# Performance work log

Hardware: AMD Instinct MI355X
Metric: run time of the kernel (lower is better)

The kernel has to match this reference:

```python
import jax, jax.numpy as jnp
import numpy as np

LAST_Q = 64      # queries used for dynamic pattern estimation (MInference default)
V_TOPK = 1024    # number of vertical (column) indices kept
S_TOPK = 2048    # number of slash (diagonal) offsets kept
FORCE_V = 30     # first columns always kept
FORCE_S = 100    # most-recent diagonals always kept


def setup_inputs() -> dict:
    key = jax.random.key(0)
    kq, kk, kv = jax.random.split(key, 3)
    B, H, S, D = 1, 8, 4096, 128
    q = jax.random.normal(kq, (B, H, S, D), dtype=jnp.float32)
    k = jax.random.normal(kk, (B, H, S, D), dtype=jnp.float32)
    v = jax.random.normal(kv, (B, H, S, D), dtype=jnp.float32)
    return {"q": q, "k": k, "v": v}


def _vertical_slash_attention(q, k, v):
    B, H, S, D = q.shape
    scale = 1.0 / np.sqrt(D).astype(np.float32)

    # ---- pattern estimation on the last LAST_Q queries ----
    qk = jnp.einsum('bhqd,bhkd->bhqk', q[:, :, -LAST_Q:], k) * scale  # [B,H,LQ,S]
    qpos = S - LAST_Q + jnp.arange(LAST_Q)                            # query positions
    causal_last = qpos[:, None] >= jnp.arange(S)[None, :]             # [LQ,S]
    qk = jnp.where(causal_last, qk, jnp.finfo(qk.dtype).min)
    qk = jax.nn.softmax(qk, axis=-1)

    # vertical (column) scores
    vertical = qk.sum(axis=2)                                         # [B,H,S]
    vertical = vertical.at[..., :FORCE_V].set(jnp.inf)
    v_idx = jax.lax.top_k(vertical, V_TOPK)[1]                        # column ids [B,H,V_TOPK]

    # slash (diagonal) scores, indexed by distance o = i - j in [0, S)
    dist = qpos[:, None] - jnp.arange(S)[None, :]                     # [LQ,S]
    dist_c = jnp.clip(dist, 0, S - 1)
    slash = jnp.zeros((B, H, S), qk.dtype).at[:, :, dist_c].add(
        jnp.where(dist >= 0, qk, 0.0))                                # [B,H,S]
    slash = slash.at[..., :FORCE_S].set(jnp.inf)
    s_off = jax.lax.top_k(slash, S_TOPK)[1]                           # diagonal offsets [B,H,S_TOPK]

    # ---- build vertical-slash sparsity mask ----
    ar = jnp.arange(S)
    v_mask = (v_idx[..., :, None] == ar).any(axis=-2)                 # [B,H,S] column allowed
    s_mask = (s_off[..., :, None] == ar).any(axis=-2)                 # [B,H,S] offset allowed

    dmat = ar[:, None] - ar[None, :]                                  # [S,S] query-key distance
    causal = dmat >= 0
    allowed = causal & (v_mask[:, :, None, :] | s_mask[:, :, jnp.clip(dmat, 0, S - 1)])

    # ---- sparse (mask-equivalent) attention ----
    scores = jnp.einsum('bhqd,bhkd->bhqk', q, k) * scale              # [B,H,S,S]
    scores = jnp.where(allowed, scores, jnp.finfo(scores.dtype).min)
    probs = jax.nn.softmax(scores, axis=-1)
    return jnp.einsum('bhqk,bhkd->bhqd', probs, v)


def reference(q, k, v):
    return _vertical_slash_attention(q, k, v)
```

## Files before the change

kernel.cpp:

```cpp
#include <hip/hip_runtime.h>
#include <hip/hip_bf16.h>
#include <math.h>

#define S_LEN 4096
#define DHEAD 128
#define NHEAD 8
#define LASTQ 64
#define V_TOPK 1024
#define S_TOPK 2048
#define FORCE_V 30
#define FORCE_S 100

#define SCALE 0.08838834764831845f
#define NEGBIG -3.0e38f

#define NJOBS 111

typedef __attribute__((ext_vector_type(8))) short short8;
typedef __attribute__((ext_vector_type(4))) float floatx4;
typedef unsigned long long u64;

__device__ __forceinline__ unsigned short f2bf(float f) {
    unsigned u = __float_as_uint(f);
    unsigned r = (u + 0x7fffu + ((u >> 16) & 1u)) >> 16;
    return (unsigned short)r;
}
__device__ __forceinline__ float bf2f(unsigned short s) {
    unsigned u = ((unsigned)s) << 16;
    return __uint_as_float(u);
}

__device__ const short jobQ[NJOBS] = {
    0,1,2,3,4, 5,5, 6,6, 7,7, 8,8, 9,9, 10,10,
    11,11,11, 12,12,12, 13,13,13, 14,14,14, 15,15,15,
    16,16,16,16, 17,17,17,17, 18,18,18,18, 19,19,19,19, 20,20,20,20, 21,21,21,21,
    22,22,22,22,22, 23,23,23,23,23, 24,24,24,24,24, 25,25,25,25,25, 26,26,26,26,26,
    27,27,27,27,27,27, 28,28,28,28,28,28, 29,29,29,29,29,29, 30,30,30,30,30,30,
    31,31,31,31,31,31};
__device__ const short jobK0[NJOBS] = {
    0,0,0,0,0, 0,6, 0,7, 0,8, 0,9, 0,10, 0,11,
    0,8,16, 0,9,18, 0,10,19, 0,10,20, 0,11,22,
    0,9,18,26, 0,9,18,27, 0,10,20,29, 0,10,20,30, 0,11,22,32, 0,11,22,33,
    0,10,19,28,37, 0,10,20,30,39, 0,10,20,30,40, 0,11,22,32,42, 0,11,22,33,44,
    0,10,20,29,38,47, 0,10,20,30,40,49, 0,10,20,30,40,50, 0,11,22,32,42,52,
    0,11,22,33,44,54};
__device__ const short jobK1[NJOBS] = {
    2,4,6,8,10, 6,12, 7,14, 8,16, 9,18, 10,20, 11,22,
    8,16,24, 9,18,26, 10,19,28, 10,20,30, 11,22,32,
    9,18,26,34, 9,18,27,36, 10,20,29,38, 10,20,30,40, 11,22,32,42, 11,22,33,44,
    10,19,28,37,46, 10,20,30,39,48, 10,20,30,40,50, 11,22,32,42,52, 11,22,33,44,54,
    10,20,29,38,47,56, 10,20,30,40,49,58, 10,20,30,40,50,60, 11,22,32,42,52,62,
    11,22,33,44,54,64};
__device__ const short pBase[32] = {0,1,2,3,4,5,7,9,11,13,15,17,20,23,26,29,
                                    32,36,40,44,48,52,56,61,66,71,76,81,87,93,99,105};
__device__ const short pCnt[32]  = {1,1,1,1,1,2,2,2,2,2,2,3,3,3,3,3,
                                    4,4,4,4,4,4,5,5,5,5,5,6,6,6,6,6};

__global__ __launch_bounds__(256) void prep_score(const float* __restrict__ q,
                                                  const float* __restrict__ k,
                                                  const float* __restrict__ v,
                                                  unsigned short* __restrict__ kbf,
                                                  unsigned short* __restrict__ vtbf,
                                                  float* __restrict__ scores) {
    int b = blockIdx.x, t = threadIdx.x;
    __shared__ __align__(16) float4 SH[64 * 32];

    if (b < 512) {
        const float4* src = (const float4*)k;
        int base = b * 2048;
#pragma unroll
        for (int i = 0; i < 8; ++i) {
            int idx = base + i * 256 + t;
            float4 val = src[idx];
            ushort4 o;
            o.x = f2bf(val.x); o.y = f2bf(val.y); o.z = f2bf(val.z); o.w = f2bf(val.w);
            ((ushort4*)kbf)[idx] = o;
        }
    } else if (b < 1536) {
        int bx = b - 512;
        int h  = bx >> 7;
        int rem = bx & 127;
        int d0 = (rem >> 6) * 64;
        int k0 = (rem & 63) * 64;
        unsigned short (*T)[72] = reinterpret_cast<unsigned short(*)[72]>(SH);
#pragma unroll
        for (int it = 0; it < 4; ++it) {
            int idx = t + it * 256;
            int r = idx >> 4, c4 = idx & 15;
            float4 val = *(const float4*)(v + ((size_t)(h * S_LEN) + k0 + r) * DHEAD + d0 + c4 * 4);
            T[c4 * 4 + 0][r] = f2bf(val.x);
            T[c4 * 4 + 1][r] = f2bf(val.y);
            T[c4 * 4 + 2][r] = f2bf(val.z);
            T[c4 * 4 + 3][r] = f2bf(val.w);
        }
        __syncthreads();
#pragma unroll
        for (int it = 0; it < 2; ++it) {
            int idx = t + it * 256;
            int r = idx >> 3, c8 = idx & 7;
            *(uint4*)(vtbf + ((size_t)h * DHEAD + d0 + r) * S_LEN + k0 + c8 * 8) = *(uint4*)&T[r][c8 * 8];
        }
    } else {
        int bx = b - 1536;
        int h  = bx >> 6;
        int kt = bx & 63;
        int jl = t >> 2, part = t & 3;
        int j  = kt * 64 + jl;

        float4* Qs = (float4*)SH;
        const float4* qbase = (const float4*)(q + ((size_t)h * S_LEN + (S_LEN - LASTQ)) * DHEAD);
        for (int idx = t; idx < 64 * 32; idx += 256) Qs[idx] = qbase[idx];
        __syncthreads();

        float4 kr[8];
        const float4* kp = (const float4*)(k + ((size_t)h * S_LEN + j) * DHEAD) + part * 8;
#pragma unroll
        for (int c = 0; c < 8; ++c) kr[c] = kp[c];

        float* sp = scores + (size_t)h * LASTQ * S_LEN + j;
#pragma unroll 4
        for (int qi = 0; qi < LASTQ; ++qi) {
            const float4* qp4 = Qs + qi * 32 + part * 8;
            float dot = 0.f;
#pragma unroll
            for (int c = 0; c < 8; ++c) {
                float4 a = qp4[c], bb = kr[c];
                dot += a.x * bb.x + a.y * bb.y + a.z * bb.z + a.w * bb.w;
            }
            dot += __shfl_xor(dot, 1, 64);
            dot += __shfl_xor(dot, 2, 64);
            if (part == 0) {
                int qpos = S_LEN - LASTQ + qi;
                sp[(size_t)qi * S_LEN] = (j <= qpos) ? dot * SCALE : NEGBIG;
            }
        }
    }
}

__global__ __launch_bounds__(256) void row_stats(const float* __restrict__ scores,
                                                 float* __restrict__ m_out,
                                                 float* __restrict__ inv_out) {
    int row  = blockIdx.x * 4 + (threadIdx.x >> 6);
    int lane = threadIdx.x & 63;
    const float4* rp = (const float4*)(scores + (size_t)row * S_LEN);
    float mx = NEGBIG;
    for (int i = lane; i < S_LEN / 4; i += 64) {
        float4 s4 = rp[i];
        mx = fmaxf(mx, fmaxf(fmaxf(s4.x, s4.y), fmaxf(s4.z, s4.w)));
    }
#pragma unroll
    for (int d = 32; d >= 1; d >>= 1) mx = fmaxf(mx, __shfl_xor(mx, d, 64));
    float su = 0.f;
    for (int i = lane; i < S_LEN / 4; i += 64) {
        float4 s4 = rp[i];
        su += __expf(s4.x - mx) + __expf(s4.y - mx) + __expf(s4.z - mx) + __expf(s4.w - mx);
    }
#pragma unroll
    for (int d = 32; d >= 1; d >>= 1) su += __shfl_xor(su, d, 64);
    if (lane == 0) { m_out[row] = mx; inv_out[row] = 1.0f / su; }
}

__global__ __launch_bounds__(1024) void pattern_finish(const float* __restrict__ scores,
                                                       const float* __restrict__ m_all,
                                                       const float* __restrict__ inv_all,
                                                       unsigned* __restrict__ col_mask,
                                                       unsigned* __restrict__ diag_mask) {
    int h   = blockIdx.x >> 1;
    int sel = blockIdx.x & 1;
    int t = threadIdx.x;
    int kwant  = sel ? S_TOPK : V_TOPK;
    int forced = sel ? FORCE_S : FORCE_V;
    unsigned* dst = sel ? (diag_mask + h * 128) : (col_mask + h * 128);

    __shared__ float sm[LASTQ], sv[LASTQ];
    __shared__ unsigned keys[S_LEN];
    __shared__ int hist[256];
    __shared__ int sh_digit, sh_want;

    if (t < LASTQ) { sm[t] = m_all[h * LASTQ + t]; sv[t] = inv_all[h * LASTQ + t]; }
    __syncthreads();

    const float* S0 = scores + (size_t)h * LASTQ * S_LEN;
#pragma unroll
    for (int rep = 0; rep < 4; ++rep) {
        int j = rep * 1024 + t;
        float acc = 0.f;
        if (sel == 0) {
            for (int r = 0; r < LASTQ; ++r)
                acc += __expf(S0[(size_t)r * S_LEN + j] - sm[r]) * sv[r];
        } else {
            for (int r = 0; r < LASTQ; ++r) {
                int idx = (S_LEN - LASTQ) + r - j;
                if (idx >= 0)
                    acc += __expf(S0[(size_t)r * S_LEN + idx] - sm[r]) * sv[r];
            }
        }
        float f = (j < forced) ? __builtin_inff() : acc;
        unsigned u = __float_as_uint(f);
        u = (u & 0x80000000u) ? ~u : (u | 0x80000000u);
        keys[j] = u;
    }
    __syncthreads();

    unsigned prefix = 0;
    int want = kwant;
    for (int shift = 24; shift >= 0; shift -= 8) {
        if (t < 256) hist[t] = 0;
        __syncthreads();
        for (int j = t; j < S_LEN; j += 1024) {
            unsigned key = keys[j];
            bool match = (shift == 24) || (((key ^ prefix) >> (shift + 8)) == 0);
            if (match) atomicAdd(&hist[(key >> shift) & 255u], 1);
        }
        __syncthreads();
        if (t == 0) {
            int cum = 0, d = 255;
            for (; d >= 0; --d) {
                cum += hist[d];
                if (cum >= want) break;
            }
            sh_digit = d;
            sh_want  = want - (cum - hist[d]);
        }
        __syncthreads();
        prefix |= ((unsigned)sh_digit) << shift;
        want = sh_want;
        __syncthreads();
    }
    if (t < 128) {
        unsigned bits = 0;
        for (int b = 0; b < 32; ++b)
            if (keys[t * 32 + b] >= prefix) bits |= (1u << b);
        dst[t] = bits;
    }
}

#define PS_STRIDE 72

__global__ __launch_bounds__(256, 2) void sparse_attn_mfma(
        const float* __restrict__ q,
        const unsigned short* __restrict__ kbf,
        const unsigned short* __restrict__ vtbf,
        const unsigned* __restrict__ col_mask,
        const unsigned* __restrict__ diag_mask,
        unsigned short* __restrict__ pO, float* __restrict__ pm, float* __restrict__ pl) {
    int b = blockIdx.x;
    int h = b & 7;
    int job = b >> 3;
    int Q  = jobQ[job];
    int k0 = jobK0[job];
    int k1 = jobK1[job];
    int i0 = Q * 128;
    int t    = threadIdx.x;
    int wave = t >> 6;
    int lane = t & 63;
    int ln16 = lane & 15;
    int quad = lane >> 4;
    int lsw  = ln16 & 7;

    __shared__ __align__(16) unsigned short Ks[64 * 128];
    __shared__ __align__(16) unsigned short Vt[128 * 64];
    __shared__ __align__(16) unsigned short Ps[8 * 16 * PS_STRIDE];
    __shared__ u64 allowed[128];
    __shared__ unsigned dmLDS[130];

    if (t < 130) dmLDS[t] = (t < 128) ? diag_mask[h * 128 + t] : 0u;

    const int ti0 = t, ti1 = t + 256, ti2 = t + 512, ti3 = t + 768;
    const int kgo0 = (ti0 >> 4) * DHEAD + (ti0 & 15) * 8;
    const int kgo1 = (ti1 >> 4) * DHEAD + (ti1 & 15) * 8;
    const int kgo2 = (ti2 >> 4) * DHEAD + (ti2 & 15) * 8;
    const int kgo3 = (ti3 >> 4) * DHEAD + (ti3 & 15) * 8;
    const int kso0 = (ti0 >> 4) * 128 + (((ti0 & 15) ^ ((ti0 >> 4) & 7)) << 3);
    const int kso1 = (ti1 >> 4) * 128 + (((ti1 & 15) ^ ((ti1 >> 4) & 7)) << 3);
    const int kso2 = (ti2 >> 4) * 128 + (((ti2 & 15) ^ ((ti2 >> 4) & 7)) << 3);
    const int kso3 = (ti3 >> 4) * 128 + (((ti3 & 15) ^ ((ti3 >> 4) & 7)) << 3);
    const int vgo0 = (ti0 >> 3) * S_LEN + (ti0 & 7) * 8;
    const int vgo1 = (ti1 >> 3) * S_LEN + (ti1 & 7) * 8;
    const int vgo2 = (ti2 >> 3) * S_LEN + (ti2 & 7) * 8;
    const int vgo3 = (ti3 >> 3) * S_LEN + (ti3 & 7) * 8;
    const int vso0 = (ti0 >> 3) * 64 + (((ti0 & 7) ^ ((ti0 >> 3) & 7)) << 3);
    const int vso1 = (ti1 >> 3) * 64 + (((ti1 & 7) ^ ((ti1 >> 3) & 7)) << 3);
    const int vso2 = (ti2 >> 3) * 64 + (((ti2 & 7) ^ ((ti2 >> 3) & 7)) << 3);
    const int vso3 = (ti3 >> 3) * 64 + (((ti3 & 7) ^ ((ti3 >> 3) & 7)) << 3);

    short8 qf[2][4];
#pragma unroll
    for (int s = 0; s < 2; ++s) {
        int qrow = i0 + wave * 32 + s * 16 + ln16;
        const float* qp = q + ((size_t)h * S_LEN + qrow) * DHEAD;
#pragma unroll
        for (int ds = 0; ds < 4; ++ds) {
            int base = ds * 32 + quad * 8;
            float4 a = *(const float4*)(qp + base);
            float4 c = *(const float4*)(qp + base + 4);
            union { unsigned short u[8]; short8 v; } tmp;
            tmp.u[0] = f2bf(a.x * SCALE); tmp.u[1] = f2bf(a.y * SCALE);
            tmp.u[2] = f2bf(a.z * SCALE); tmp.u[3] = f2bf(a.w * SCALE);
            tmp.u[4] = f2bf(c.x * SCALE); tmp.u[5] = f2bf(c.y * SCALE);
            tmp.u[6] = f2bf(c.z * SCALE); tmp.u[7] = f2bf(c.w * SCALE);
            qf[s][ds] = tmp.v;
        }
    }

    floatx4 o4[2][8];
#pragma unroll
    for (int s = 0; s < 2; ++s)
#pragma unroll
        for (int n = 0; n < 8; ++n) o4[s][n] = (floatx4){0.f, 0.f, 0.f, 0.f};
    float m_run[2][4] = {{NEGBIG, NEGBIG, NEGBIG, NEGBIG}, {NEGBIG, NEGBIG, NEGBIG, NEGBIG}};
    float l_run[2][4] = {{0.f, 0.f, 0.f, 0.f}, {0.f, 0.f, 0.f, 0.f}};

    unsigned short* psw[2];
    psw[0] = Ps + (wave * 2 + 0) * 16 * PS_STRIDE;
    psw[1] = Ps + (wave * 2 + 1) * 16 * PS_STRIDE;

    const unsigned short* kgbase = kbf + (size_t)h * S_LEN * DHEAD;
    const unsigned short* vgbase = vtbf + (size_t)h * DHEAD * S_LEN;

    uint4 ka0, ka1, ka2, ka3, va0, va1, va2, va3;
    {
        const unsigned short* kg = kgbase + (size_t)(k0 * 64) * DHEAD;
        const unsigned short* vg = vgbase + k0 * 64;
        ka0 = *(const uint4*)(kg + kgo0); ka1 = *(const uint4*)(kg + kgo1);
        ka2 = *(const uint4*)(kg + kgo2); ka3 = *(const uint4*)(kg + kgo3);
        va0 = *(const uint4*)(vg + vgo0); va1 = *(const uint4*)(vg + vgo1);
        va2 = *(const uint4*)(vg + vgo2); va3 = *(const uint4*)(vg + vgo3);
    }

    for (int jt = k0; jt < k1; ++jt) {
        int j0 = jt * 64;
        __syncthreads();

        *(uint4*)&Ks[kso0] = ka0; *(uint4*)&Ks[kso1] = ka1;
        *(uint4*)&Ks[kso2] = ka2; *(uint4*)&Ks[kso3] = ka3;
        *(uint4*)&Vt[vso0] = va0; *(uint4*)&Vt[vso1] = va1;
        *(uint4*)&Vt[vso2] = va2; *(uint4*)&Vt[vso3] = va3;

        if (jt + 1 < k1) {
            const unsigned short* kg = kgbase + (size_t)(j0 + 64) * DHEAD;
            const unsigned short* vg = vgbase + (j0 + 64);
            ka0 = *(const uint4*)(kg + kgo0); ka1 = *(const uint4*)(kg + kgo1);
            ka2 = *(const uint4*)(kg + kgo2); ka3 = *(const uint4*)(kg + kgo3);
            va0 = *(const uint4*)(vg + vgo0); va1 = *(const uint4*)(vg + vgo1);
            va2 = *(const uint4*)(vg + vgo2); va3 = *(const uint4*)(vg + vgo3);
        }

        if (t < 128) {
            int i = i0 + t;
            int off0 = i - j0;
            u64 a = 0;
            if (off0 >= 0) {
                u64 causal = (off0 >= 63) ? ~0ull : ((1ull << (off0 + 1)) - 1ull);
                u64 cwv = ((u64)col_mask[h * 128 + (j0 >> 5) + 1] << 32) |
                          (u64)col_mask[h * 128 + (j0 >> 5)];
                int sb = off0 - 63;
                u64 V;
                if (sb >= 0) {
                    int w = sb >> 5, sh = sb & 31;
                    u64 lo = ((u64)dmLDS[w + 1] << 32) | (u64)dmLDS[w];
                    u64 hi = (u64)dmLDS[w + 2];
                    V = (lo >> sh) | (sh ? (hi << (64 - sh)) : 0ull);
                } else {
                    u64 w0 = ((u64)dmLDS[1] << 32) | (u64)dmLDS[0];
                    V = w0 << (-sb);
                }
                a = (cwv | __brevll(V)) & causal;
            }
            allowed[t] = a;
        }
        __syncthreads();

        floatx4 sa[2][4];
#pragma unroll
        for (int s = 0; s < 2; ++s)
#pragma unroll
            for (int c = 0; c < 4; ++c) sa[s][c] = (floatx4){0.f, 0.f, 0.f, 0.f};
        __builtin_amdgcn_s_setprio(1);
#pragma unroll
        for (int c = 0; c < 4; ++c) {
            const unsigned short* kbase = Ks + (c * 16 + ln16) * 128;
#pragma unroll
            for (int ds = 0; ds < 4; ++ds) {
                short8 kf = *(const short8*)(kbase + (((ds * 4 + quad) ^ lsw) << 3));
                sa[0][c] = __builtin_amdgcn_mfma_f32_16x16x32_bf16(qf[0][ds], kf, sa[0][c], 0, 0, 0);
                sa[1][c] = __builtin_amdgcn_mfma_f32_16x16x32_bf16(qf[1][ds], kf, sa[1][c], 0, 0, 0);
            }
        }
        __builtin_amdgcn_s_setprio(0);

#pragma unroll
        for (int s = 0; s < 2; ++s) {
            u64 ash[4];
#pragma unroll
            for (int r = 0; r < 4; ++r)
                ash[r] = allowed[wave * 32 + s * 16 + quad * 4 + r] >> ln16;
            float sc[4][4];
#pragma unroll
            for (int c = 0; c < 4; ++c)
#pragma unroll
                for (int r = 0; r < 4; ++r) {
                    bool ok = (ash[r] >> (c * 16)) & 1ull;
                    sc[c][r] = ok ? sa[s][c][r] : -__builtin_inff();
                }
            float mloc[4];
#pragma unroll
            for (int r = 0; r < 4; ++r) {
                float mx = fmaxf(fmaxf(sc[0][r], sc[1][r]), fmaxf(sc[2][r], sc[3][r]));
#pragma unroll
                for (int d = 8; d >= 1; d >>= 1) mx = fmaxf(mx, __shfl_xor(mx, d, 64));
                mloc[r] = mx;
            }
            bool nd = (mloc[0] > m_run[s][0]) | (mloc[1] > m_run[s][1]) |
                      (mloc[2] > m_run[s][2]) | (mloc[3] > m_run[s][3]);
            if (__any((int)nd)) {
#pragma unroll
                for (int r = 0; r < 4; ++r) {
                    float mn = fmaxf(m_run[s][r], mloc[r]);
                    float al = __expf(m_run[s][r] - mn);
                    m_run[s][r] = mn;
                    l_run[s][r] *= al;
#pragma unroll
                    for (int n = 0; n < 8; ++n) o4[s][n][r] *= al;
                }
            }
#pragma unroll
            for (int r = 0; r < 4; ++r) {
                float su = 0.f;
                float pvr[4];
#pragma unroll
                for (int c = 0; c < 4; ++c) {
                    float p = __expf(sc[c][r] - m_run[s][r]);
                    pvr[c] = p;
                    su += p;
                }
#pragma unroll
                for (int c = 0; c < 4; ++c)
                    psw[s][(quad * 4 + r) * PS_STRIDE + c * 16 + ln16] = f2bf(pvr[c]);
#pragma unroll
                for (int d = 8; d >= 1; d >>= 1) su += __shfl_xor(su, d, 64);
                l_run[s][r] += su;
            }
        }
        asm volatile("" ::: "memory");

        short8 pf[2][2];
#pragma unroll
        for (int s = 0; s < 2; ++s) {
            pf[s][0] = *(const short8*)&psw[s][ln16 * PS_STRIDE + quad * 8];
            pf[s][1] = *(const short8*)&psw[s][ln16 * PS_STRIDE + 32 + quad * 8];
        }

        __builtin_amdgcn_s_setprio(1);
#pragma unroll
        for (int n = 0; n < 8; ++n) {
            const unsigned short* vbase = Vt + (n * 16 + ln16) * 64;
            short8 vf0 = *(const short8*)(vbase + ((quad ^ lsw) << 3));
            short8 vf1 = *(const short8*)(vbase + (((quad + 4) ^ lsw) << 3));
            o4[0][n] = __builtin_amdgcn_mfma_f32_16x16x32_bf16(pf[0][0], vf0, o4[0][n], 0, 0, 0);
            o4[0][n] = __builtin_amdgcn_mfma_f32_16x16x32_bf16(pf[0][1], vf1, o4[0][n], 0, 0, 0);
            o4[1][n] = __builtin_amdgcn_mfma_f32_16x16x32_bf16(pf[1][0], vf0, o4[1][n], 0, 0, 0);
            o4[1][n] = __builtin_amdgcn_mfma_f32_16x16x32_bf16(pf[1][1], vf1, o4[1][n], 0, 0, 0);
        }
        __builtin_amdgcn_s_setprio(0);
    }

    int pidx = h * NJOBS + job;
    unsigned short* pOp = pO + (size_t)pidx * (128 * DHEAD);
#pragma unroll
    for (int s = 0; s < 2; ++s)
#pragma unroll
        for (int r = 0; r < 4; ++r) {
            int row = wave * 32 + s * 16 + quad * 4 + r;
            if (ln16 == 0) {
                pm[pidx * 128 + row] = m_run[s][r];
                pl[pidx * 128 + row] = l_run[s][r];
            }
#pragma unroll
            for (int n = 0; n < 8; ++n)
                pOp[row * DHEAD + n * 16 + ln16] = f2bf(o4[s][n][r]);
        }
}

__global__ __launch_bounds__(256) void merge_out(const unsigned short* __restrict__ pO,
                                                 const float* __restrict__ pm,
                                                 const float* __restrict__ pl,
                                                 float* __restrict__ out) {
    int b = blockIdx.x;
    int h = b >> 5, Q = b & 31;
    int t = threadIdx.x;
    int row = t >> 1, half = t & 1;
    int p0 = h * NJOBS + pBase[Q];
    int cnt = pCnt[Q];

    float mp[6], lp[6];
    float ms = NEGBIG;
    for (int p = 0; p < cnt; ++p) {
        mp[p] = pm[(p0 + p) * 128 + row];
        lp[p] = pl[(p0 + p) * 128 + row];
        ms = fmaxf(ms, mp[p]);
    }
    float denom = 0.f, w[6];
    for (int p = 0; p < cnt; ++p) {
        w[p] = __expf(mp[p] - ms);
        denom += w[p] * lp[p];
    }
    float invl = 1.0f / denom;

    float acc[64];
#pragma unroll
    for (int i = 0; i < 64; ++i) acc[i] = 0.f;
    for (int p = 0; p < cnt; ++p) {
        const unsigned short* Op = pO + (size_t)(p0 + p) * (128 * DHEAD) + row * DHEAD + half * 64;
        float wp = w[p];
#pragma unroll
        for (int g = 0; g < 8; ++g) {
            ushort4 u0 = ((const ushort4*)Op)[g * 2];
            ushort4 u1 = ((const ushort4*)Op)[g * 2 + 1];
            acc[g * 8 + 0] += wp * bf2f(u0.x); acc[g * 8 + 1] += wp * bf2f(u0.y);
            acc[g * 8 + 2] += wp * bf2f(u0.z); acc[g * 8 + 3] += wp * bf2f(u0.w);
            acc[g * 8 + 4] += wp * bf2f(u1.x); acc[g * 8 + 5] += wp * bf2f(u1.y);
            acc[g * 8 + 6] += wp * bf2f(u1.z); acc[g * 8 + 7] += wp * bf2f(u1.w);
        }
    }
    float* op = out + ((size_t)h * S_LEN + Q * 128 + row) * DHEAD + half * 64;
#pragma unroll
    for (int g = 0; g < 16; ++g) {
        float4 c;
        c.x = acc[g * 4 + 0] * invl; c.y = acc[g * 4 + 1] * invl;
        c.z = acc[g * 4 + 2] * invl; c.w = acc[g * 4 + 3] * invl;
        ((float4*)op)[g] = c;
    }
}

extern "C" void kernel_launch(void* const* d_in, const int* in_sizes, int n_in,
                              void* d_out, int out_size, void* d_ws, size_t ws_size,
                              hipStream_t stream) {
    const float* q = (const float*)d_in[0];
    const float* k = (const float*)d_in[1];
    const float* v = (const float*)d_in[2];
    float* out = (float*)d_out;

    unsigned* col_m  = (unsigned*)d_ws;
    unsigned* diag_m = col_m + 1024;
    float* m_all   = (float*)(diag_m + 1024);
    float* inv_all = m_all + 512;
    unsigned short* kbf  = (unsigned short*)(inv_all + 512);
    unsigned short* vtbf = kbf + (size_t)NHEAD * S_LEN * DHEAD;
    float* scores = (float*)(vtbf + (size_t)NHEAD * S_LEN * DHEAD);
    unsigned short* pO = (unsigned short*)(scores + (size_t)NHEAD * LASTQ * S_LEN);
    float* pm = (float*)(pO + (size_t)8 * NJOBS * 128 * DHEAD);
    float* pl = pm + 8 * NJOBS * 128;

    prep_score<<<2048, 256, 0, stream>>>(q, k, v, kbf, vtbf, scores);
    row_stats<<<NHEAD * LASTQ / 4, 256, 0, stream>>>(scores, m_all, inv_all);
    pattern_finish<<<NHEAD * 2, 1024, 0, stream>>>(scores, m_all, inv_all, col_m, diag_m);
    sparse_attn_mfma<<<NHEAD * NJOBS, 256, 0, stream>>>(q, kbf, vtbf, col_m, diag_m, pO, pm, pl);
    merge_out<<<NHEAD * 32, 256, 0, stream>>>(pO, pm, pl, out);
}
```

Measured before the change: 308.7 us.

## Transpose QK MFMA so each lane owns a query row, cutting softmax shuffles

Swaps the MFMA operands for QK^T so the score tile is transposed and each lane holds one query row. Row max and sum then need only two cross-quad shuffles instead of four-step butterflies per row. Probabilities are packed with v_cvt_pk_bf16 and written to an XOR-swizzled LDS tile. The change also removes the register prefetch of the next K/V tile, loading directly into LDS each iteration, and drops the s_setprio hints. This lowers register pressure and ALU work, at the cost of exposing global-load latency, and the alpha rescale now needs extra broadcast shuffles.

```diff
diff --git a/kernel.cpp b/kernel.cpp
--- a/kernel.cpp
+++ b/kernel.cpp
@@ -28,6 +28,11 @@
 __device__ __forceinline__ float bf2f(unsigned short s) {
     unsigned u = ((unsigned)s) << 16;
     return __uint_as_float(u);
+}
+__device__ __forceinline__ unsigned cvt_pk_bf16(float lo, float hi) {
+    unsigned d;
+    asm("v_cvt_pk_bf16_f32 %0, %1, %2" : "=v"(d) : "v"(lo), "v"(hi));
+    return d;
 }
 
 __device__ const short jobQ[NJOBS] = {
@@ -235,8 +240,6 @@
     }
 }
 
-#define PS_STRIDE 72
-
 __global__ __launch_bounds__(256, 2) void sparse_attn_mfma(
         const float* __restrict__ q,
         const unsigned short* __restrict__ kbf,
@@ -260,7 +263,7 @@
 
     __shared__ __align__(16) unsigned short Ks[64 * 128];
     __shared__ __align__(16) unsigned short Vt[128 * 64];
-    __shared__ __align__(16) unsigned short Ps[8 * 16 * PS_STRIDE];
+    __shared__ __align__(16) unsigned short Ps[8][1024];
     __shared__ u64 allowed[128];
     __shared__ unsigned dmLDS[130];
 
@@ -308,44 +311,31 @@
     for (int s = 0; s < 2; ++s)
 #pragma unroll
         for (int n = 0; n < 8; ++n) o4[s][n] = (floatx4){0.f, 0.f, 0.f, 0.f};
-    float m_run[2][4] = {{NEGBIG, NEGBIG, NEGBIG, NEGBIG}, {NEGBIG, NEGBIG, NEGBIG, NEGBIG}};
-    float l_run[2][4] = {{0.f, 0.f, 0.f, 0.f}, {0.f, 0.f, 0.f, 0.f}};
-
-    unsigned short* psw[2];
-    psw[0] = Ps + (wave * 2 + 0) * 16 * PS_STRIDE;
-    psw[1] = Ps + (wave * 2 + 1) * 16 * PS_STRIDE;
+    float m_run[2] = {NEGBIG, NEGBIG};
+    float l_run[2] = {0.f, 0.f};
+
+    unsigned short* ps0 = &Ps[wave * 2 + 0][0];
+    unsigned short* ps1 = &Ps[wave * 2 + 1][0];
 
     const unsigned short* kgbase = kbf + (size_t)h * S_LEN * DHEAD;
     const unsigned short* vgbase = vtbf + (size_t)h * DHEAD * S_LEN;
 
-    uint4 ka0, ka1, ka2, ka3, va0, va1, va2, va3;
-    {
-        const unsigned short* kg = kgbase + (size_t)(k0 * 64) * DHEAD;
-        const unsigned short* vg = vgbase + k0 * 64;
-        ka0 = *(const uint4*)(kg + kgo0); ka1 = *(const uint4*)(kg + kgo1);
-        ka2 = *(const uint4*)(kg + kgo2); ka3 = *(const uint4*)(kg + kgo3);
-        va0 = *(const uint4*)(vg + vgo0); va1 = *(const uint4*)(vg + vgo1);
-        va2 = *(const uint4*)(vg + vgo2); va3 = *(const uint4*)(vg + vgo3);
-    }
-
     for (int jt = k0; jt < k1; ++jt) {
         int j0 = jt * 64;
         __syncthreads();
 
-        *(uint4*)&Ks[kso0] = ka0; *(uint4*)&Ks[kso1] = ka1;
-        *(uint4*)&Ks[kso2] = ka2; *(uint4*)&Ks[kso3] = ka3;
-        *(uint4*)&Vt[vso0] = va0; *(uint4*)&Vt[vso1] = va1;
-        *(uint4*)&Vt[vso2] = va2; *(uint4*)&Vt[vso3] = va3;
-
-        if (jt + 1 < k1) {
-            const unsigned short* kg = kgbase + (size_t)(j0 + 64) * DHEAD;
-            const unsigned short* vg = vgbase + (j0 + 64);
-            ka0 = *(const uint4*)(kg + kgo0); ka1 = *(const uint4*)(kg + kgo1);
-            ka2 = *(const uint4*)(kg + kgo2); ka3 = *(const uint4*)(kg + kgo3);
-            va0 = *(const uint4*)(vg + vgo0); va1 = *(const uint4*)(vg + vgo1);
-            va2 = *(const uint4*)(vg + vgo2); va3 = *(const uint4*)(vg + vgo3);
-        }
-
+        {
+            const unsigned short* kg = kgbase + (size_t)j0 * DHEAD;
+            const unsigned short* vg = vgbase + j0;
+            *(uint4*)&Ks[kso0] = *(const uint4*)(kg + kgo0);
+            *(uint4*)&Ks[kso1] = *(const uint4*)(kg + kgo1);
+            *(uint4*)&Ks[kso2] = *(const uint4*)(kg + kgo2);
+            *(uint4*)&Ks[kso3] = *(const uint4*)(kg + kgo3);
+            *(uint4*)&Vt[vso0] = *(const uint4*)(vg + vgo0);
+            *(uint4*)&Vt[vso1] = *(const uint4*)(vg + vgo1);
+            *(uint4*)&Vt[vso2] = *(const uint4*)(vg + vgo2);
+            *(uint4*)&Vt[vso3] = *(const uint4*)(vg + vgo3);
+        }
         if (t < 128) {
             int i = i0 + t;
             int off0 = i - j0;
@@ -376,82 +366,84 @@
         for (int s = 0; s < 2; ++s)
 #pragma unroll
             for (int c = 0; c < 4; ++c) sa[s][c] = (floatx4){0.f, 0.f, 0.f, 0.f};
-        __builtin_amdgcn_s_setprio(1);
 #pragma unroll
         for (int c = 0; c < 4; ++c) {
             const unsigned short* kbase = Ks + (c * 16 + ln16) * 128;
 #pragma unroll
             for (int ds = 0; ds < 4; ++ds) {
                 short8 kf = *(const short8*)(kbase + (((ds * 4 + quad) ^ lsw) << 3));
-                sa[0][c] = __builtin_amdgcn_mfma_f32_16x16x32_bf16(qf[0][ds], kf, sa[0][c], 0, 0, 0);
-                sa[1][c] = __builtin_amdgcn_mfma_f32_16x16x32_bf16(qf[1][ds], kf, sa[1][c], 0, 0, 0);
-            }
-        }
-        __builtin_amdgcn_s_setprio(0);
+                sa[0][c] = __builtin_amdgcn_mfma_f32_16x16x32_bf16(kf, qf[0][ds], sa[0][c], 0, 0, 0);
+                sa[1][c] = __builtin_amdgcn_mfma_f32_16x16x32_bf16(kf, qf[1][ds], sa[1][c], 0, 0, 0);
+            }
+        }
 
 #pragma unroll
         for (int s = 0; s < 2; ++s) {
-            u64 ash[4];
-#pragma unroll
-            for (int r = 0; r < 4; ++r)
-                ash[r] = allowed[wave * 32 + s * 16 + quad * 4 + r] >> ln16;
+            u64 A = allowed[wave * 32 + s * 16 + ln16];
             float sc[4][4];
 #pragma unroll
-            for (int c = 0; c < 4; ++c)
-#pragma unroll
-                for (int r = 0; r < 4; ++r) {
-                    bool ok = (ash[r] >> (c * 16)) & 1ull;
-                    sc[c][r] = ok ? sa[s][c][r] : -__builtin_inff();
+            for (int c = 0; c < 4; ++c) {
+                unsigned nib = (unsigned)(A >> (c * 16 + quad * 4)) & 15u;
+#pragma unroll
+                for (int r = 0; r < 4; ++r)
+                    sc[c][r] = (nib & (1u << r)) ? sa[s][c][r] : -__builtin_inff();
+            }
+            float mx = fmaxf(
+                fmaxf(fmaxf(fmaxf(sc[0][0], sc[0][1]), fmaxf(sc[0][2], sc[0][3])),
+                      fmaxf(fmaxf(sc[1][0], sc[1][1]), fmaxf(sc[1][2], sc[1][3]))),
+                fmaxf(fmaxf(fmaxf(sc[2][0], sc[2][1]), fmaxf(sc[2][2], sc[2][3])),
+                      fmaxf(fmaxf(sc[3][0], sc[3][1]), fmaxf(sc[3][2], sc[3][3]))));
+            mx = fmaxf(mx, __shfl_xor(mx, 16, 64));
+            mx = fmaxf(mx, __shfl_xor(mx, 32, 64));
+            bool nd = mx > m_run[s];
+            if (__any((int)nd)) {
+                float mn = fmaxf(m_run[s], mx);
+                float al = __expf(m_run[s] - mn);
+                m_run[s] = mn;
+                l_run[s] *= al;
+                float a0 = __shfl(al, quad * 4 + 0, 64);
+                float a1 = __shfl(al, quad * 4 + 1, 64);
+                float a2 = __shfl(al, quad * 4 + 2, 64);
+                float a3 = __shfl(al, quad * 4 + 3, 64);
+#pragma unroll
+                for (int n = 0; n < 8; ++n) {
+                    o4[s][n][0] *= a0; o4[s][n][1] *= a1;
+                    o4[s][n][2] *= a2; o4[s][n][3] *= a3;
                 }
-            float mloc[4];
-#pragma unroll
-            for (int r = 0; r < 4; ++r) {
-                float mx = fmaxf(fmaxf(sc[0][r], sc[1][r]), fmaxf(sc[2][r], sc[3][r]));
-#pragma unroll
-                for (int d = 8; d >= 1; d >>= 1) mx = fmaxf(mx, __shfl_xor(mx, d, 64));
-                mloc[r] = mx;
-            }
-            bool nd = (mloc[0] > m_run[s][0]) | (mloc[1] > m_run[s][1]) |
-                      (mloc[2] > m_run[s][2]) | (mloc[3] > m_run[s][3]);
-            if (__any((int)nd)) {
-#pragma unroll
-                for (int r = 0; r < 4; ++r) {
-                    float mn = fmaxf(m_run[s][r], mloc[r]);
-                    float al = __expf(m_run[s][r] - mn);
-                    m_run[s][r] = mn;
-                    l_run[s][r] *= al;
-#pragma unroll
-                    for (int n = 0; n < 8; ++n) o4[s][n][r] *= al;
-                }
-            }
-#pragma unroll
-            for (int r = 0; r < 4; ++r) {
-                float su = 0.f;
-                float pvr[4];
-#pragma unroll
-                for (int c = 0; c < 4; ++c) {
-                    float p = __expf(sc[c][r] - m_run[s][r]);
-                    pvr[c] = p;
-                    su += p;
-                }
-#pragma unroll
-                for (int c = 0; c < 4; ++c)
-                    psw[s][(quad * 4 + r) * PS_STRIDE + c * 16 + ln16] = f2bf(pvr[c]);
-#pragma unroll
-                for (int d = 8; d >= 1; d >>= 1) su += __shfl_xor(su, d, 64);
-                l_run[s][r] += su;
-            }
+            }
+            unsigned short* psb = s ? ps1 : ps0;
+            float su = 0.f;
+#pragma unroll
+            for (int c = 0; c < 4; ++c) {
+                float p0 = __expf(sc[c][0] - m_run[s]);
+                float p1 = __expf(sc[c][1] - m_run[s]);
+                float p2 = __expf(sc[c][2] - m_run[s]);
+                float p3 = __expf(sc[c][3] - m_run[s]);
+                su += (p0 + p1) + (p2 + p3);
+                unsigned d0 = cvt_pk_bf16(p0, p1);
+                unsigned d1 = cvt_pk_bf16(p2, p3);
+                *(u64*)&psb[ln16 * 64 + (((c * 4 + quad) ^ ln16) << 2)] =
+                    ((u64)d1 << 32) | (u64)d0;
+            }
+            su += __shfl_xor(su, 16, 64);
+            su += __shfl_xor(su, 32, 64);
+            l_run[s] += su;
         }
         asm volatile("" ::: "memory");
 
         short8 pf[2][2];
 #pragma unroll
         for (int s = 0; s < 2; ++s) {
-            pf[s][0] = *(const short8*)&psw[s][ln16 * PS_STRIDE + quad * 8];
-            pf[s][1] = *(const short8*)&psw[s][ln16 * PS_STRIDE + 32 + quad * 8];
-        }
-
-        __builtin_amdgcn_s_setprio(1);
+            const unsigned short* psb = s ? ps1 : ps0;
+            union { u64 qq[2]; short8 v; } pk0, pk1;
+            pk0.qq[0] = *(const u64*)&psb[ln16 * 64 + (((quad * 2 + 0) ^ ln16) << 2)];
+            pk0.qq[1] = *(const u64*)&psb[ln16 * 64 + (((quad * 2 + 1) ^ ln16) << 2)];
+            pk1.qq[0] = *(const u64*)&psb[ln16 * 64 + (((8 + quad * 2 + 0) ^ ln16) << 2)];
+            pk1.qq[1] = *(const u64*)&psb[ln16 * 64 + (((8 + quad * 2 + 1) ^ ln16) << 2)];
+            pf[s][0] = pk0.v;
+            pf[s][1] = pk1.v;
+        }
+
 #pragma unroll
         for (int n = 0; n < 8; ++n) {
             const unsigned short* vbase = Vt + (n * 16 + ln16) * 64;
@@ -462,24 +454,25 @@
             o4[1][n] = __builtin_amdgcn_mfma_f32_16x16x32_bf16(pf[1][0], vf0, o4[1][n], 0, 0, 0);
             o4[1][n] = __builtin_amdgcn_mfma_f32_16x16x32_bf16(pf[1][1], vf1, o4[1][n], 0, 0, 0);
         }
-        __builtin_amdgcn_s_setprio(0);
     }
 
     int pidx = h * NJOBS + job;
     unsigned short* pOp = pO + (size_t)pidx * (128 * DHEAD);
 #pragma unroll
-    for (int s = 0; s < 2; ++s)
+    for (int s = 0; s < 2; ++s) {
+        if (quad == 0) {
+            int row = wave * 32 + s * 16 + ln16;
+            pm[pidx * 128 + row] = m_run[s];
+            pl[pidx * 128 + row] = l_run[s];
+        }
 #pragma unroll
         for (int r = 0; r < 4; ++r) {
             int row = wave * 32 + s * 16 + quad * 4 + r;
-            if (ln16 == 0) {
-                pm[pidx * 128 + row] = m_run[s][r];
-                pl[pidx * 128 + row] = l_run[s][r];
-            }
 #pragma unroll
             for (int n = 0; n < 8; ++n)
                 pOp[row * DHEAD + n * 16 + ln16] = f2bf(o4[s][n][r]);
         }
+    }
 }
 
 __global__ __launch_bounds__(256) void merge_out(const unsigned short* __restrict__ pO,
```

Result: no change. 310.9 us (+0.7%).
